# Optimization experiments

Measured on AMD Instinct MI355X. Metric: run time of the kernel, lower is better.

Reference implementation:

```python
import jax, jax.numpy as jnp
import numpy as np

B, N, H, A, O = 32, 1024, 256, 32, 256
RESAMPLE_THRESHOLD = 0.5
EPS = 1e-10


def setup_inputs() -> dict:
    key = jax.random.key(0)
    ks = jax.random.split(key, 16)
    s = 0.05  # small weight scale (stands in for xavier init, keeps softmax sane)
    w = jax.random.uniform(ks[1], (B, N), jnp.float32)
    return {
        "particles": jax.random.normal(ks[0], (B, N, H), jnp.float32),
        "weights": w / jnp.sum(w, axis=1, keepdims=True),
        "action": jax.random.normal(ks[2], (B, A), jnp.float32),
        "observation": jax.random.normal(ks[3], (B, O), jnp.float32),
        "u": jax.random.uniform(ks[4], (B, 1), jnp.float32),
        "Wr": jax.random.normal(ks[5], (H + A, H), jnp.float32) * s,
        "br": jnp.zeros((H,), jnp.float32),
        "Wu": jax.random.normal(ks[6], (H + A, H), jnp.float32) * s,
        "bu": jnp.zeros((H,), jnp.float32),
        "Wc": jax.random.normal(ks[7], (H + A, H), jnp.float32) * s,
        "bc": jnp.zeros((H,), jnp.float32),
        "W0": jax.random.normal(ks[8], (H + O, H), jnp.float32) * s,
        "b0": jnp.zeros((H,), jnp.float32),
        "W1": jax.random.normal(ks[9], (H, H), jnp.float32) * s,
        "b1": jnp.zeros((H,), jnp.float32),
        "W2": jax.random.normal(ks[10], (H, 1), jnp.float32) * s,
        "b2": jnp.zeros((1,), jnp.float32),
    }


def reference(particles, weights, action, observation, u,
              Wr, br, Wu, bu, Wc, bc, W0, b0, W1, b1, W2, b2):
    b, n, h = particles.shape
    act = jnp.broadcast_to(action[:, None, :], (b, n, action.shape[-1]))
    obs = jnp.broadcast_to(observation[:, None, :], (b, n, observation.shape[-1]))

    # --- GRU-style transition (stochastic head is dead code in update()) ---
    x = jnp.concatenate([particles, act], axis=-1)            # [B,N,H+A]
    reset = jax.nn.sigmoid(x @ Wr + br)
    update = jax.nn.sigmoid(x @ Wu + bu)
    x_reset = jnp.concatenate([particles * reset, act], axis=-1)
    cand = jnp.tanh(x_reset @ Wc + bc)
    nxt = (1.0 - update) * particles + update * cand          # [B,N,H]

    # --- observation log-likelihood MLP ---
    z = jnp.concatenate([nxt, obs], axis=-1)                  # [B,N,H+O]
    z = jax.nn.gelu(z @ W0 + b0, approximate=False)
    z = jax.nn.gelu(z @ W1 + b1, approximate=False)
    log_lik = (z @ W2 + b2)[..., 0]                           # [B,N]

    # --- weight update (stable softmax) ---
    log_w = jnp.log(weights + EPS) + log_lik
    log_w = log_w - jnp.max(log_w, axis=1, keepdims=True)
    new_w = jax.nn.softmax(log_w, axis=1)                     # [B,N]

    ess = 1.0 / (jnp.sum(new_w * new_w, axis=1) + EPS)        # [B]
    should = ess < RESAMPLE_THRESHOLD * n                     # [B] bool

    # --- systematic resampling (computed for all rows, selected by mask) ---
    csum = jnp.cumsum(new_w, axis=1)                          # [B,N]
    pos = u / n + jnp.arange(n, dtype=jnp.float32) / n        # [B,N]
    pos = jnp.minimum(pos, 0.9999)
    idx = jax.vmap(jnp.searchsorted)(csum, pos)               # [B,N]
    idx = jnp.clip(idx, 0, n - 1)
    resampled = jnp.take_along_axis(nxt, idx[..., None], axis=1)
    uniform_w = jnp.full_like(new_w, 1.0 / n)

    nxt = jnp.where(should[:, None, None], resampled, nxt)
    new_w = jnp.where(should[:, None], uniform_w, new_w)

    belief = jnp.sum(nxt * new_w[..., None], axis=1)          # [B,H]
    return belief, nxt, new_w, ess
```

## Files before the change

kernel.cpp:

```cpp
#include <hip/hip_runtime.h>
#include <math.h>

#define B_ 32
#define N_ 1024
#define H_ 256
#define A_ 32
#define O_ 256
#define M_ (B_*N_)
#define EPSF 1e-10f

typedef _Float16 f16;
typedef __attribute__((ext_vector_type(8))) _Float16 f16x8;
typedef __attribute__((ext_vector_type(4))) _Float16 f16x4;
typedef __attribute__((ext_vector_type(4))) float    f32x4;

__device__ __forceinline__ float gelu_exact(float x){
  return 0.5f * x * (1.0f + erff(x * 0.70710678118654752f));
}
__device__ __forceinline__ float sigm(float x){
  return 1.0f / (1.0f + expf(-x));
}

__global__ __launch_bounds__(256) void k_tw(
    const float* __restrict__ Wr, const float* __restrict__ Wu,
    const float* __restrict__ Wc, const float* __restrict__ W0,
    const float* __restrict__ W1,
    f16* __restrict__ WrT, f16* __restrict__ WuT, f16* __restrict__ WcT,
    f16* __restrict__ W0T, f16* __restrict__ W1T)
{
  __shared__ float tile[64][65];
  const int mat = blockIdx.y;
  const int kb  = (blockIdx.x >> 2) * 64;
  const int nb  = (blockIdx.x & 3) * 64;
  const float* W; f16* WT;
  switch (mat) {
    case 0: W = Wr; WT = WrT; break;
    case 1: W = Wu; WT = WuT; break;
    case 2: W = Wc; WT = WcT; break;
    case 3: W = W0; WT = W0T; break;
    default: W = W1; WT = W1T; break;
  }
  const int t = threadIdx.x;
  const int c = t & 63, r4 = t >> 6;
  #pragma unroll
  for (int i = 0; i < 64; i += 4)
    tile[i + r4][c] = W[(size_t)(kb + i + r4)*H_ + nb + c];
  __syncthreads();
  #pragma unroll
  for (int i = 0; i < 64; i += 4)
    WT[(size_t)(nb + i + r4)*H_ + kb + c] = (f16)tile[c][i + r4];
}

__global__ __launch_bounds__(256) void k_pre(
    const float* __restrict__ action, const float* __restrict__ observation,
    const float* __restrict__ Wr, const float* __restrict__ br,
    const float* __restrict__ Wu, const float* __restrict__ bu,
    const float* __restrict__ Wc, const float* __restrict__ bc,
    const float* __restrict__ W0, const float* __restrict__ b0,
    float* __restrict__ actR, float* __restrict__ actU,
    float* __restrict__ actC, float* __restrict__ obs0)
{
  int b = blockIdx.x, j = threadIdx.x;
  float aR = br[j], aU = bu[j], aC = bc[j];
  for (int a = 0; a < A_; ++a) {
    float av = action[b*A_ + a];
    aR = fmaf(av, Wr[(H_+a)*H_ + j], aR);
    aU = fmaf(av, Wu[(H_+a)*H_ + j], aU);
    aC = fmaf(av, Wc[(H_+a)*H_ + j], aC);
  }
  float o0 = b0[j];
  for (int o = 0; o < O_; ++o)
    o0 = fmaf(observation[b*O_ + o], W0[(H_+o)*H_ + j], o0);
  actR[b*H_+j] = aR; actU[b*H_+j] = aU; actC[b*H_+j] = aC; obs0[b*H_+j] = o0;
}

__device__ __forceinline__ f16x8 lda(const unsigned char* xs, int m, int kt,
                                     int lr, int lg, int aswz) {
  int off = (((m*16 + lr)*512) + kt*64 + lg*16) ^ aswz;
  return *(const f16x8*)(xs + off);
}

__device__ __forceinline__ void gemm256(const unsigned char* xs, const f16* __restrict__ Wt,
                                        int lr, int lg, int aswz, int colbase,
                                        f32x4 acc[4][4]) {
  for (int kt = 0; kt < 8; ++kt) {
    f16x8 a[4], bb[4];
    #pragma unroll
    for (int m = 0; m < 4; ++m) a[m] = lda(xs, m, kt, lr, lg, aswz);
    #pragma unroll
    for (int n = 0; n < 4; ++n)
      bb[n] = *(const f16x8*)(Wt + (size_t)(colbase + n*16 + lr)*H_ + kt*32 + lg*8);
    #pragma unroll
    for (int m = 0; m < 4; ++m)
      #pragma unroll
      for (int n = 0; n < 4; ++n)
        acc[m][n] = __builtin_amdgcn_mfma_f32_16x16x32_f16(a[m], bb[n], acc[m][n], 0, 0, 0);
  }
}

__device__ __forceinline__ void xs_w16(unsigned char* xs, int row, int col, f16 v) {
  int off = (row*512 + col*2) ^ ((row&7)<<4);
  *(f16*)(xs + off) = v;
}

__global__ __launch_bounds__(256, 2) void k_gru_mlp(
    const float* __restrict__ particles, const float* __restrict__ weights,
    const f16* __restrict__ WrT, const f16* __restrict__ WuT,
    const f16* __restrict__ WcT, const f16* __restrict__ W0T,
    const f16* __restrict__ W1T,
    const float* __restrict__ W2, const float* __restrict__ b1v,
    const float* __restrict__ b2v,
    const float* __restrict__ actR, const float* __restrict__ actU,
    const float* __restrict__ actC, const float* __restrict__ obs0,
    float* __restrict__ ws_nxt, float* __restrict__ log_w)
{
  __shared__ __align__(16) unsigned char xs[64*512];
  __shared__ float red[4][64];

  const int b    = blockIdx.x >> 4;
  const int n0   = (blockIdx.x & 15) << 6;
  const int tid  = threadIdx.x;
  const int w    = tid >> 6;
  const int lane = tid & 63;
  const int lr   = lane & 15;
  const int lg   = lane >> 4;
  const int aswz = (lr & 7) << 4;
  const int colbase = w << 6;
  const float* Pbase = particles + (size_t)(b*N_ + n0) * H_;

  int colv[4];
  #pragma unroll
  for (int n = 0; n < 4; ++n) colv[n] = colbase + n*16 + lr;

  #pragma unroll
  for (int i = 0; i < 8; ++i) {
    int s = tid + i*256;
    int row = s >> 5, ks = s & 31;
    const float* src = Pbase + row*H_ + ks*8;
    float4 v0 = *(const float4*)src;
    float4 v1 = *(const float4*)(src + 4);
    f16x8 h;
    h[0]=(f16)v0.x; h[1]=(f16)v0.y; h[2]=(f16)v0.z; h[3]=(f16)v0.w;
    h[4]=(f16)v1.x; h[5]=(f16)v1.y; h[6]=(f16)v1.z; h[7]=(f16)v1.w;
    int off = (row*512 + ks*16) ^ ((row&7)<<4);
    *(f16x8*)(xs + off) = h;
  }
  __syncthreads();

  f32x4 aR[4][4];
  #pragma unroll
  for (int m=0;m<4;++m)
    #pragma unroll
    for (int n=0;n<4;++n) aR[m][n] = (f32x4)(0.f);
  gemm256(xs, WrT, lr, lg, aswz, colbase, aR);

  f32x4 aU[4][4];
  #pragma unroll
  for (int m=0;m<4;++m)
    #pragma unroll
    for (int n=0;n<4;++n) aU[m][n] = (f32x4)(0.f);
  gemm256(xs, WuT, lr, lg, aswz, colbase, aU);

  float vR[4], vU[4];
  #pragma unroll
  for (int n=0;n<4;++n) { vR[n] = actR[b*H_ + colv[n]]; vU[n] = actU[b*H_ + colv[n]]; }

  f16x4 uh[4][4];
  #pragma unroll
  for (int m=0;m<4;++m)
    #pragma unroll
    for (int n=0;n<4;++n)
      #pragma unroll
      for (int r=0;r<4;++r) {
        aR[m][n][r] = sigm(aR[m][n][r] + vR[n]);
        uh[m][n][r] = (f16)sigm(aU[m][n][r] + vU[n]);
      }

  __syncthreads();

  #pragma unroll
  for (int m=0;m<4;++m)
    #pragma unroll
    for (int n=0;n<4;++n)
      #pragma unroll
      for (int r=0;r<4;++r) {
        int row = m*16 + lg*4 + r;
        float orig = Pbase[row*H_ + colv[n]];
        xs_w16(xs, row, colv[n], (f16)(orig * aR[m][n][r]));
      }
  __syncthreads();

  f32x4 aC[4][4];
  #pragma unroll
  for (int m=0;m<4;++m)
    #pragma unroll
    for (int n=0;n<4;++n) aC[m][n] = (f32x4)(0.f);
  gemm256(xs, WcT, lr, lg, aswz, colbase, aC);

  float vC[4];
  #pragma unroll
  for (int n=0;n<4;++n) vC[n] = actC[b*H_ + colv[n]];

  #pragma unroll
  for (int m=0;m<4;++m)
    #pragma unroll
    for (int n=0;n<4;++n)
      #pragma unroll
      for (int r=0;r<4;++r) {
        int row = m*16 + lg*4 + r;
        float cand = tanhf(aC[m][n][r] + vC[n]);
        float orig = Pbase[row*H_ + colv[n]];
        float uu   = (float)uh[m][n][r];
        float nx   = fmaf(uu, cand - orig, orig);
        aC[m][n][r] = nx;
        ws_nxt[(size_t)(b*N_ + n0 + row)*H_ + colv[n]] = nx;
      }
  __syncthreads();
  #pragma unroll
  for (int m=0;m<4;++m)
    #pragma unroll
    for (int n=0;n<4;++n)
      #pragma unroll
      for (int r=0;r<4;++r)
        xs_w16(xs, m*16 + lg*4 + r, colv[n], (f16)aC[m][n][r]);
  __syncthreads();

  f32x4 a0[4][4];
  #pragma unroll
  for (int m=0;m<4;++m)
    #pragma unroll
    for (int n=0;n<4;++n) a0[m][n] = (f32x4)(0.f);
  gemm256(xs, W0T, lr, lg, aswz, colbase, a0);

  float v0b[4];
  #pragma unroll
  for (int n=0;n<4;++n) v0b[n] = obs0[b*H_ + colv[n]];
  #pragma unroll
  for (int m=0;m<4;++m)
    #pragma unroll
    for (int n=0;n<4;++n)
      #pragma unroll
      for (int r=0;r<4;++r)
        a0[m][n][r] = gelu_exact(a0[m][n][r] + v0b[n]);
  __syncthreads();
  #pragma unroll
  for (int m=0;m<4;++m)
    #pragma unroll
    for (int n=0;n<4;++n)
      #pragma unroll
      for (int r=0;r<4;++r)
        xs_w16(xs, m*16 + lg*4 + r, colv[n], (f16)a0[m][n][r]);
  __syncthreads();

  f32x4 a1[4][4];
  #pragma unroll
  for (int m=0;m<4;++m)
    #pragma unroll
    for (int n=0;n<4;++n) a1[m][n] = (f32x4)(0.f);
  gemm256(xs, W1T, lr, lg, aswz, colbase, a1);

  float v1b[4], w2v[4];
  #pragma unroll
  for (int n=0;n<4;++n) { v1b[n] = b1v[colv[n]]; w2v[n] = W2[colv[n]]; }

  float psum[4][4];
  #pragma unroll
  for (int m=0;m<4;++m)
    #pragma unroll
    for (int r=0;r<4;++r) psum[m][r] = 0.f;
  #pragma unroll
  for (int m=0;m<4;++m)
    #pragma unroll
    for (int n=0;n<4;++n)
      #pragma unroll
      for (int r=0;r<4;++r)
        psum[m][r] = fmaf(gelu_exact(a1[m][n][r] + v1b[n]), w2v[n], psum[m][r]);

  #pragma unroll
  for (int m=0;m<4;++m)
    #pragma unroll
    for (int r=0;r<4;++r) {
      float v = psum[m][r];
      v += __shfl_xor(v, 1); v += __shfl_xor(v, 2);
      v += __shfl_xor(v, 4); v += __shfl_xor(v, 8);
      psum[m][r] = v;
    }
  if (lr == 0) {
    #pragma unroll
    for (int m=0;m<4;++m)
      #pragma unroll
      for (int r=0;r<4;++r)
        red[w][m*16 + lg*4 + r] = psum[m][r];
  }
  __syncthreads();
  if (tid < 64) {
    float ll = red[0][tid] + red[1][tid] + red[2][tid] + red[3][tid] + b2v[0];
    int gi = b*N_ + n0 + tid;
    log_w[gi] = logf(weights[gi] + EPSF) + ll;
  }
}

__global__ __launch_bounds__(256) void k_softmax(
    const float* __restrict__ log_w, const float* __restrict__ u_in,
    float* __restrict__ d_new_w, float* __restrict__ d_ess,
    int* __restrict__ ws_idx, float* __restrict__ ws_should)
{
  __shared__ float cs[N_];
  __shared__ float part[256];
  __shared__ float redbuf[4];
  const int b = blockIdx.x, t = threadIdx.x;
  const int wave = t >> 6, lane = t & 63;
  const float* lw = log_w + b*N_;

  float v[4];
  float m = -INFINITY;
  #pragma unroll
  for (int q = 0; q < 4; ++q) { v[q] = lw[t*4+q]; m = fmaxf(m, v[q]); }
  for (int off = 32; off >= 1; off >>= 1) m = fmaxf(m, __shfl_xor(m, off));
  if (lane == 0) redbuf[wave] = m;
  __syncthreads();
  m = fmaxf(fmaxf(redbuf[0], redbuf[1]), fmaxf(redbuf[2], redbuf[3]));

  float s4 = 0.f;
  #pragma unroll
  for (int q = 0; q < 4; ++q) { v[q] = expf(v[q] - m); s4 += v[q]; }
  part[t] = s4;
  __syncthreads();
  for (int off = 1; off < 256; off <<= 1) {
    float pv = (t >= off) ? part[t-off] : 0.f;
    __syncthreads();
    part[t] += pv;
    __syncthreads();
  }
  const float total = part[255];
  const float excl  = part[t] - s4;
  const float inv   = 1.0f / total;

  float run = excl, sq4 = 0.f;
  #pragma unroll
  for (int q = 0; q < 4; ++q) {
    run += v[q];
    cs[t*4+q] = run * inv;
    float wq = v[q] * inv;
    sq4 += wq * wq;
  }
  for (int off = 32; off >= 1; off >>= 1) sq4 += __shfl_xor(sq4, off);
  __syncthreads();
  if (lane == 0) redbuf[wave] = sq4;
  __syncthreads();
  const float ssq = redbuf[0] + redbuf[1] + redbuf[2] + redbuf[3];
  const float ess = 1.0f / (ssq + EPSF);
  const bool should = ess < (0.5f * (float)N_);
  if (t == 0) { d_ess[b] = ess; ws_should[b] = should ? 1.0f : 0.0f; }

  const float uw = 1.0f / (float)N_;
  #pragma unroll
  for (int q = 0; q < 4; ++q)
    d_new_w[b*N_ + t*4+q] = should ? uw : v[q] * inv;

  const float ub = u_in[b];
  #pragma unroll
  for (int q = 0; q < 4; ++q) {
    int i = t*4 + q;
    float pos = fminf(ub / (float)N_ + (float)i / (float)N_, 0.9999f);
    int lo = 0, hi = N_;
    while (lo < hi) { int mid = (lo + hi) >> 1; if (cs[mid] < pos) lo = mid + 1; else hi = mid; }
    ws_idx[b*N_ + i] = (lo < N_-1) ? lo : N_-1;
  }
}

#define TMF 32
__global__ __launch_bounds__(256) void k_final(
    const float* __restrict__ ws_nxt, const int* __restrict__ ws_idx,
    const float* __restrict__ ws_should, const float* __restrict__ d_new_w,
    float* __restrict__ d_nxt, float* __restrict__ d_belief)
{
  const int blk = blockIdx.x;
  const int b  = blk >> 5;
  const int n0 = (blk & 31) * TMF;
  const int j  = threadIdx.x;
  const bool should = ws_should[b] != 0.0f;
  float partial = 0.f;
  for (int p = 0; p < TMF; ++p) {
    int n = n0 + p;
    int src = should ? ws_idx[b*N_ + n] : n;
    float vv = ws_nxt[((size_t)(b*N_ + src))*H_ + j];
    d_nxt[((size_t)(b*N_ + n))*H_ + j] = vv;
    partial = fmaf(vv, d_new_w[b*N_ + n], partial);
  }
  atomicAdd(&d_belief[b*H_ + j], partial);
}

extern "C" void kernel_launch(void* const* d_in, const int* in_sizes, int n_in,
                              void* d_out, int out_size, void* d_ws, size_t ws_size,
                              hipStream_t stream) {
  (void)in_sizes; (void)n_in; (void)out_size; (void)ws_size;
  const float* particles   = (const float*)d_in[0];
  const float* weights     = (const float*)d_in[1];
  const float* action      = (const float*)d_in[2];
  const float* observation = (const float*)d_in[3];
  const float* u_in        = (const float*)d_in[4];
  const float* Wr = (const float*)d_in[5];
  const float* br = (const float*)d_in[6];
  const float* Wu = (const float*)d_in[7];
  const float* bu = (const float*)d_in[8];
  const float* Wc = (const float*)d_in[9];
  const float* bc = (const float*)d_in[10];
  const float* W0 = (const float*)d_in[11];
  const float* b0 = (const float*)d_in[12];
  const float* W1 = (const float*)d_in[13];
  const float* b1 = (const float*)d_in[14];
  const float* W2 = (const float*)d_in[15];
  const float* b2 = (const float*)d_in[16];

  float* out      = (float*)d_out;
  float* d_belief = out;
  float* d_nxt    = out + (size_t)B_*H_;
  float* d_new_w  = d_nxt + (size_t)M_*H_;
  float* d_ess    = d_new_w + M_;

  unsigned char* wsb = (unsigned char*)d_ws;
  f16* WrT = (f16*)wsb;
  f16* WuT = WrT + H_*H_;
  f16* WcT = WuT + H_*H_;
  f16* W0T = WcT + H_*H_;
  f16* W1T = W0T + H_*H_;
  float* ws_nxt   = (float*)(W1T + H_*H_);
  float* ws_logw  = ws_nxt + (size_t)M_*H_;
  float* ws_actR  = ws_logw + M_;
  float* ws_actU  = ws_actR + B_*H_;
  float* ws_actC  = ws_actU + B_*H_;
  float* ws_obs0  = ws_actC + B_*H_;
  int*   ws_idx   = (int*)(ws_obs0 + B_*H_);
  float* ws_should= (float*)(ws_idx + M_);

  hipMemsetAsync(d_belief, 0, (size_t)B_*H_*sizeof(float), stream);

  k_tw<<<dim3(16, 5), dim3(256), 0, stream>>>(
      Wr, Wu, Wc, W0, W1, WrT, WuT, WcT, W0T, W1T);

  k_pre<<<dim3(B_), dim3(256), 0, stream>>>(
      action, observation, Wr, br, Wu, bu, Wc, bc, W0, b0,
      ws_actR, ws_actU, ws_actC, ws_obs0);

  k_gru_mlp<<<dim3(M_/64), dim3(256), 0, stream>>>(
      particles, weights, WrT, WuT, WcT, W0T, W1T, W2, b1, b2,
      ws_actR, ws_actU, ws_actC, ws_obs0, ws_nxt, ws_logw);

  k_softmax<<<dim3(B_), dim3(256), 0, stream>>>(
      ws_logw, u_in, d_new_w, d_ess, ws_idx, ws_should);

  k_final<<<dim3(M_/TMF), dim3(256), 0, stream>>>(
      ws_nxt, ws_idx, ws_should, d_new_w, d_nxt, d_belief);
}
```

Measured before the change: 280.5 us.

## Store intermediate particles in fp16, fuse prep kernels, shuffle-based scan

Merges the weight-transpose and bias-precompute kernels into one launch. The GRU kernel now reads the original particles from the fp16 shared tile instead of re-reading global fp32. It writes the next-state particles to the workspace as fp16 using coalesced 16-byte stores, which halves intermediate traffic. Occupancy is raised to 3 blocks per SM, the softmax prefix sum uses wave shuffles instead of a barrier-heavy shared scan, and the final gather kernel is vectorized. The cost is reduced precision: the nxt output now round-trips through fp16, which may change results beyond tolerance.

```diff
diff --git a/kernel.cpp b/kernel.cpp
--- a/kernel.cpp
+++ b/kernel.cpp
@@ -12,6 +12,7 @@
 typedef _Float16 f16;
 typedef __attribute__((ext_vector_type(8))) _Float16 f16x8;
 typedef __attribute__((ext_vector_type(4))) _Float16 f16x4;
+typedef __attribute__((ext_vector_type(2))) _Float16 f16x2;
 typedef __attribute__((ext_vector_type(4))) float    f32x4;
 
 __device__ __forceinline__ float gelu_exact(float x){
@@ -21,72 +22,78 @@
   return 1.0f / (1.0f + expf(-x));
 }
 
-__global__ __launch_bounds__(256) void k_tw(
-    const float* __restrict__ Wr, const float* __restrict__ Wu,
-    const float* __restrict__ Wc, const float* __restrict__ W0,
-    const float* __restrict__ W1,
-    f16* __restrict__ WrT, f16* __restrict__ WuT, f16* __restrict__ WcT,
-    f16* __restrict__ W0T, f16* __restrict__ W1T)
-{
-  __shared__ float tile[64][65];
-  const int mat = blockIdx.y;
-  const int kb  = (blockIdx.x >> 2) * 64;
-  const int nb  = (blockIdx.x & 3) * 64;
-  const float* W; f16* WT;
-  switch (mat) {
-    case 0: W = Wr; WT = WrT; break;
-    case 1: W = Wu; WT = WuT; break;
-    case 2: W = Wc; WT = WcT; break;
-    case 3: W = W0; WT = W0T; break;
-    default: W = W1; WT = W1T; break;
-  }
-  const int t = threadIdx.x;
-  const int c = t & 63, r4 = t >> 6;
-  #pragma unroll
-  for (int i = 0; i < 64; i += 4)
-    tile[i + r4][c] = W[(size_t)(kb + i + r4)*H_ + nb + c];
-  __syncthreads();
-  #pragma unroll
-  for (int i = 0; i < 64; i += 4)
-    WT[(size_t)(nb + i + r4)*H_ + kb + c] = (f16)tile[c][i + r4];
-}
-
-__global__ __launch_bounds__(256) void k_pre(
+__global__ __launch_bounds__(256) void k_prep(
     const float* __restrict__ action, const float* __restrict__ observation,
     const float* __restrict__ Wr, const float* __restrict__ br,
     const float* __restrict__ Wu, const float* __restrict__ bu,
     const float* __restrict__ Wc, const float* __restrict__ bc,
     const float* __restrict__ W0, const float* __restrict__ b0,
+    f16* __restrict__ WrT, f16* __restrict__ WuT, f16* __restrict__ WcT,
+    f16* __restrict__ W0T, f16* __restrict__ W1T, const float* __restrict__ W1,
     float* __restrict__ actR, float* __restrict__ actU,
     float* __restrict__ actC, float* __restrict__ obs0)
 {
-  int b = blockIdx.x, j = threadIdx.x;
-  float aR = br[j], aU = bu[j], aC = bc[j];
-  for (int a = 0; a < A_; ++a) {
-    float av = action[b*A_ + a];
-    aR = fmaf(av, Wr[(H_+a)*H_ + j], aR);
-    aU = fmaf(av, Wu[(H_+a)*H_ + j], aU);
-    aC = fmaf(av, Wc[(H_+a)*H_ + j], aC);
-  }
-  float o0 = b0[j];
-  for (int o = 0; o < O_; ++o)
-    o0 = fmaf(observation[b*O_ + o], W0[(H_+o)*H_ + j], o0);
-  actR[b*H_+j] = aR; actU[b*H_+j] = aU; actC[b*H_+j] = aC; obs0[b*H_+j] = o0;
+  const int blk = blockIdx.x;
+  if (blk < 80) {
+    __shared__ float tile[64][65];
+    const int mat = blk >> 4;
+    const int kb  = ((blk & 15) >> 2) * 64;
+    const int nb  = (blk & 3) * 64;
+    const float* W; f16* WT;
+    switch (mat) {
+      case 0: W = Wr; WT = WrT; break;
+      case 1: W = Wu; WT = WuT; break;
+      case 2: W = Wc; WT = WcT; break;
+      case 3: W = W0; WT = W0T; break;
+      default: W = W1; WT = W1T; break;
+    }
+    const int t = threadIdx.x;
+    const int c = t & 63, r4 = t >> 6;
+    #pragma unroll
+    for (int i = 0; i < 64; i += 4)
+      tile[i + r4][c] = W[(size_t)(kb + i + r4)*H_ + nb + c];
+    __syncthreads();
+    #pragma unroll
+    for (int i = 0; i < 64; i += 4)
+      WT[(size_t)(nb + i + r4)*H_ + kb + c] = (f16)tile[c][i + r4];
+  } else {
+    const int b = blk - 80, j = threadIdx.x;
+    float aR = br[j], aU = bu[j], aC = bc[j];
+    for (int a = 0; a < A_; ++a) {
+      float av = action[b*A_ + a];
+      aR = fmaf(av, Wr[(H_+a)*H_ + j], aR);
+      aU = fmaf(av, Wu[(H_+a)*H_ + j], aU);
+      aC = fmaf(av, Wc[(H_+a)*H_ + j], aC);
+    }
+    float o0 = b0[j];
+    for (int o = 0; o < O_; ++o)
+      o0 = fmaf(observation[b*O_ + o], W0[(H_+o)*H_ + j], o0);
+    actR[b*H_+j] = aR; actU[b*H_+j] = aU; actC[b*H_+j] = aC; obs0[b*H_+j] = o0;
+  }
 }
 
 __device__ __forceinline__ f16x8 lda(const unsigned char* xs, int m, int kt,
-                                     int lr, int lg, int aswz) {
-  int off = (((m*16 + lr)*512) + kt*64 + lg*16) ^ aswz;
+                                     int lr, int lg) {
+  int row = m*16 + lr;
+  int off = (row*512 + kt*64 + lg*16) ^ ((row&7)<<4);
   return *(const f16x8*)(xs + off);
 }
+__device__ __forceinline__ f16 xs_r16(const unsigned char* xs, int row, int col) {
+  int off = (row*512 + col*2) ^ ((row&7)<<4);
+  return *(const f16*)(xs + off);
+}
+__device__ __forceinline__ void xs_w16(unsigned char* xs, int row, int col, f16 v) {
+  int off = (row*512 + col*2) ^ ((row&7)<<4);
+  *(f16*)(xs + off) = v;
+}
 
 __device__ __forceinline__ void gemm256(const unsigned char* xs, const f16* __restrict__ Wt,
-                                        int lr, int lg, int aswz, int colbase,
+                                        int lr, int lg, int colbase,
                                         f32x4 acc[4][4]) {
   for (int kt = 0; kt < 8; ++kt) {
     f16x8 a[4], bb[4];
     #pragma unroll
-    for (int m = 0; m < 4; ++m) a[m] = lda(xs, m, kt, lr, lg, aswz);
+    for (int m = 0; m < 4; ++m) a[m] = lda(xs, m, kt, lr, lg);
     #pragma unroll
     for (int n = 0; n < 4; ++n)
       bb[n] = *(const f16x8*)(Wt + (size_t)(colbase + n*16 + lr)*H_ + kt*32 + lg*8);
@@ -98,12 +105,7 @@
   }
 }
 
-__device__ __forceinline__ void xs_w16(unsigned char* xs, int row, int col, f16 v) {
-  int off = (row*512 + col*2) ^ ((row&7)<<4);
-  *(f16*)(xs + off) = v;
-}
-
-__global__ __launch_bounds__(256, 2) void k_gru_mlp(
+__global__ __launch_bounds__(256, 3) void k_gru_mlp(
     const float* __restrict__ particles, const float* __restrict__ weights,
     const f16* __restrict__ WrT, const f16* __restrict__ WuT,
     const f16* __restrict__ WcT, const f16* __restrict__ W0T,
@@ -112,7 +114,7 @@
     const float* __restrict__ b2v,
     const float* __restrict__ actR, const float* __restrict__ actU,
     const float* __restrict__ actC, const float* __restrict__ obs0,
-    float* __restrict__ ws_nxt, float* __restrict__ log_w)
+    f16* __restrict__ ws_nxt16, float* __restrict__ log_w)
 {
   __shared__ __align__(16) unsigned char xs[64*512];
   __shared__ float red[4][64];
@@ -124,7 +126,6 @@
   const int lane = tid & 63;
   const int lr   = lane & 15;
   const int lg   = lane >> 4;
-  const int aswz = (lr & 7) << 4;
   const int colbase = w << 6;
   const float* Pbase = particles + (size_t)(b*N_ + n0) * H_;
 
@@ -152,14 +153,14 @@
   for (int m=0;m<4;++m)
     #pragma unroll
     for (int n=0;n<4;++n) aR[m][n] = (f32x4)(0.f);
-  gemm256(xs, WrT, lr, lg, aswz, colbase, aR);
+  gemm256(xs, WrT, lr, lg, colbase, aR);
 
   f32x4 aU[4][4];
   #pragma unroll
   for (int m=0;m<4;++m)
     #pragma unroll
     for (int n=0;n<4;++n) aU[m][n] = (f32x4)(0.f);
-  gemm256(xs, WuT, lr, lg, aswz, colbase, aU);
+  gemm256(xs, WuT, lr, lg, colbase, aU);
 
   float vR[4], vU[4];
   #pragma unroll
@@ -178,6 +179,7 @@
 
   __syncthreads();
 
+  f16x4 oh[4][4];
   #pragma unroll
   for (int m=0;m<4;++m)
     #pragma unroll
@@ -185,8 +187,9 @@
       #pragma unroll
       for (int r=0;r<4;++r) {
         int row = m*16 + lg*4 + r;
-        float orig = Pbase[row*H_ + colv[n]];
-        xs_w16(xs, row, colv[n], (f16)(orig * aR[m][n][r]));
+        f16 o = xs_r16(xs, row, colv[n]);
+        oh[m][n][r] = o;
+        xs_w16(xs, row, colv[n], (f16)((float)o * aR[m][n][r]));
       }
   __syncthreads();
 
@@ -195,12 +198,13 @@
   for (int m=0;m<4;++m)
     #pragma unroll
     for (int n=0;n<4;++n) aC[m][n] = (f32x4)(0.f);
-  gemm256(xs, WcT, lr, lg, aswz, colbase, aC);
+  gemm256(xs, WcT, lr, lg, colbase, aC);
 
   float vC[4];
   #pragma unroll
   for (int n=0;n<4;++n) vC[n] = actC[b*H_ + colv[n]];
 
+  __syncthreads();
   #pragma unroll
   for (int m=0;m<4;++m)
     #pragma unroll
@@ -209,28 +213,28 @@
       for (int r=0;r<4;++r) {
         int row = m*16 + lg*4 + r;
         float cand = tanhf(aC[m][n][r] + vC[n]);
-        float orig = Pbase[row*H_ + colv[n]];
-        float uu   = (float)uh[m][n][r];
-        float nx   = fmaf(uu, cand - orig, orig);
-        aC[m][n][r] = nx;
-        ws_nxt[(size_t)(b*N_ + n0 + row)*H_ + colv[n]] = nx;
+        float orig = (float)oh[m][n][r];
+        float nx   = fmaf((float)uh[m][n][r], cand - orig, orig);
+        xs_w16(xs, row, colv[n], (f16)nx);
       }
   __syncthreads();
-  #pragma unroll
-  for (int m=0;m<4;++m)
-    #pragma unroll
-    for (int n=0;n<4;++n)
-      #pragma unroll
-      for (int r=0;r<4;++r)
-        xs_w16(xs, m*16 + lg*4 + r, colv[n], (f16)aC[m][n][r]);
-  __syncthreads();
+
+  f16* wsrow = ws_nxt16 + (size_t)(b*N_ + n0) * H_;
+  #pragma unroll
+  for (int i = 0; i < 8; ++i) {
+    int s = tid + i*256;
+    int row = s >> 5, c16 = s & 31;
+    int off = (row*512 + c16*16) ^ ((row&7)<<4);
+    f16x8 v = *(const f16x8*)(xs + off);
+    *(f16x8*)(wsrow + row*H_ + c16*8) = v;
+  }
 
   f32x4 a0[4][4];
   #pragma unroll
   for (int m=0;m<4;++m)
     #pragma unroll
     for (int n=0;n<4;++n) a0[m][n] = (f32x4)(0.f);
-  gemm256(xs, W0T, lr, lg, aswz, colbase, a0);
+  gemm256(xs, W0T, lr, lg, colbase, a0);
 
   float v0b[4];
   #pragma unroll
@@ -257,7 +261,7 @@
   for (int m=0;m<4;++m)
     #pragma unroll
     for (int n=0;n<4;++n) a1[m][n] = (f32x4)(0.f);
-  gemm256(xs, W1T, lr, lg, aswz, colbase, a1);
+  gemm256(xs, W1T, lr, lg, colbase, a1);
 
   float v1b[4], w2v[4];
   #pragma unroll
@@ -306,8 +310,8 @@
     int* __restrict__ ws_idx, float* __restrict__ ws_should)
 {
   __shared__ float cs[N_];
-  __shared__ float part[256];
   __shared__ float redbuf[4];
+  __shared__ float wsum[4];
   const int b = blockIdx.x, t = threadIdx.x;
   const int wave = t >> 6, lane = t & 63;
   const float* lw = log_w + b*N_;
@@ -324,16 +328,20 @@
   float s4 = 0.f;
   #pragma unroll
   for (int q = 0; q < 4; ++q) { v[q] = expf(v[q] - m); s4 += v[q]; }
-  part[t] = s4;
-  __syncthreads();
-  for (int off = 1; off < 256; off <<= 1) {
-    float pv = (t >= off) ? part[t-off] : 0.f;
-    __syncthreads();
-    part[t] += pv;
-    __syncthreads();
-  }
-  const float total = part[255];
-  const float excl  = part[t] - s4;
+
+  float incl = s4;
+  #pragma unroll
+  for (int off = 1; off < 64; off <<= 1) {
+    float t2 = __shfl_up(incl, off);
+    if (lane >= off) incl += t2;
+  }
+  if (lane == 63) wsum[wave] = incl;
+  __syncthreads();
+  float woff = 0.f;
+  #pragma unroll
+  for (int ww = 0; ww < 4; ++ww) woff += (ww < wave) ? wsum[ww] : 0.f;
+  const float total = wsum[0] + wsum[1] + wsum[2] + wsum[3];
+  const float excl  = woff + incl - s4;
   const float inv   = 1.0f / total;
 
   float run = excl, sq4 = 0.f;
@@ -369,26 +377,31 @@
   }
 }
 
-#define TMF 32
 __global__ __launch_bounds__(256) void k_final(
-    const float* __restrict__ ws_nxt, const int* __restrict__ ws_idx,
+    const f16* __restrict__ ws_nxt16, const int* __restrict__ ws_idx,
     const float* __restrict__ ws_should, const float* __restrict__ d_new_w,
     float* __restrict__ d_nxt, float* __restrict__ d_belief)
 {
   const int blk = blockIdx.x;
-  const int b  = blk >> 5;
-  const int n0 = (blk & 31) * TMF;
-  const int j  = threadIdx.x;
+  const int b   = blk >> 4;
+  const int n0  = (blk & 15) << 6;
+  const int t   = threadIdx.x;
+  const int c   = t & 127;
+  const int hf  = t >> 7;
   const bool should = ws_should[b] != 0.0f;
-  float partial = 0.f;
-  for (int p = 0; p < TMF; ++p) {
-    int n = n0 + p;
+  float p0 = 0.f, p1 = 0.f;
+  #pragma unroll 4
+  for (int r = 0; r < 32; ++r) {
+    int n = n0 + hf*32 + r;
     int src = should ? ws_idx[b*N_ + n] : n;
-    float vv = ws_nxt[((size_t)(b*N_ + src))*H_ + j];
-    d_nxt[((size_t)(b*N_ + n))*H_ + j] = vv;
-    partial = fmaf(vv, d_new_w[b*N_ + n], partial);
-  }
-  atomicAdd(&d_belief[b*H_ + j], partial);
+    f16x2 v = *(const f16x2*)(ws_nxt16 + (size_t)(b*N_ + src)*H_ + c*2);
+    float w = d_new_w[b*N_ + n];
+    float2 st; st.x = (float)v[0]; st.y = (float)v[1];
+    *(float2*)(d_nxt + (size_t)(b*N_ + n)*H_ + c*2) = st;
+    p0 = fmaf(st.x, w, p0); p1 = fmaf(st.y, w, p1);
+  }
+  atomicAdd(&d_belief[b*H_ + c*2],     p0);
+  atomicAdd(&d_belief[b*H_ + c*2 + 1], p1);
 }
 
 extern "C" void kernel_launch(void* const* d_in, const int* in_sizes, int n_in,
@@ -425,8 +438,8 @@
   f16* WcT = WuT + H_*H_;
   f16* W0T = WcT + H_*H_;
   f16* W1T = W0T + H_*H_;
-  float* ws_nxt   = (float*)(W1T + H_*H_);
-  float* ws_logw  = ws_nxt + (size_t)M_*H_;
+  f16* ws_nxt16   = W1T + H_*H_;
+  float* ws_logw  = (float*)(ws_nxt16 + (size_t)M_*H_);
   float* ws_actR  = ws_logw + M_;
   float* ws_actU  = ws_actR + B_*H_;
   float* ws_actC  = ws_actU + B_*H_;
@@ -436,20 +449,18 @@
 
   hipMemsetAsync(d_belief, 0, (size_t)B_*H_*sizeof(float), stream);
 
-  k_tw<<<dim3(16, 5), dim3(256), 0, stream>>>(
-      Wr, Wu, Wc, W0, W1, WrT, WuT, WcT, W0T, W1T);
-
-  k_pre<<<dim3(B_), dim3(256), 0, stream>>>(
+  k_prep<<<dim3(112), dim3(256), 0, stream>>>(
       action, observation, Wr, br, Wu, bu, Wc, bc, W0, b0,
+      WrT, WuT, WcT, W0T, W1T, W1,
       ws_actR, ws_actU, ws_actC, ws_obs0);
 
   k_gru_mlp<<<dim3(M_/64), dim3(256), 0, stream>>>(
       particles, weights, WrT, WuT, WcT, W0T, W1T, W2, b1, b2,
-      ws_actR, ws_actU, ws_actC, ws_obs0, ws_nxt, ws_logw);
+      ws_actR, ws_actU, ws_actC, ws_obs0, ws_nxt16, ws_logw);
 
   k_softmax<<<dim3(B_), dim3(256), 0, stream>>>(
       ws_logw, u_in, d_new_w, d_ess, ws_idx, ws_should);
 
-  k_final<<<dim3(M_/TMF), dim3(256), 0, stream>>>(
-      ws_nxt, ws_idx, ws_should, d_new_w, d_nxt, d_belief);
-}
+  k_final<<<dim3(M_/64), dim3(256), 0, stream>>>(
+      ws_nxt16, ws_idx, ws_should, d_new_w, d_nxt, d_belief);
+}
```

New measurement: 487.7 us. +73.9%, slower.
